# Kernel optimization log

Hardware: AMD Instinct MI355X
Metric: run time of the kernel (lower is better)

The kernel has to match this reference:

```python
import itertools
import jax, jax.numpy as jnp
import numpy as np

B, RES, RES_, STRIDE = 512, 14, 7, 2
IN_DIM, OUT_DIM, KEY_DIM, H, ATTN_RATIO = 256, 512, 16, 8, 2
NH_KD = KEY_DIM * H          # 128
D = ATTN_RATIO * KEY_DIM     # 32
DH = D * H                   # 256
KV_OUT = DH + NH_KD          # 384
N, N_ = RES * RES, RES_ * RES_   # 196, 49
EPS = 1e-5
SCALE = KEY_DIM ** -0.5


def _build_bias_idxs():
    points = list(itertools.product(range(RES), range(RES)))
    points_ = list(itertools.product(range(RES_), range(RES_)))
    offsets, idxs = {}, []
    for p1 in points_:
        for p2 in points:
            off = (abs(p1[0] * STRIDE - p2[0]), abs(p1[1] * STRIDE - p2[1]))
            if off not in offsets:
                offsets[off] = len(offsets)
            idxs.append(offsets[off])
    return np.array(idxs, dtype=np.int32).reshape(N_, N), len(offsets)


def _bn(x, g, b, m, v):
    # inference-mode BatchNorm1d over last dim
    return (x - m) * (g * jax.lax.rsqrt(v + EPS)) + b


def _hardswish(x):
    return x * jnp.clip(x + 3.0, 0.0, 6.0) * (1.0 / 6.0)


def setup_inputs() -> dict:
    key = jax.random.key(0)
    ks = jax.random.split(key, 16)
    idxs_np, n_off = _build_bias_idxs()
    inp = {
        "x": jax.random.normal(ks[0], (B, N, IN_DIM), jnp.float32),
        "w_kv": jax.random.normal(ks[1], (KV_OUT, IN_DIM), jnp.float32) * 0.02,
        "kv_g": jnp.ones((KV_OUT,), jnp.float32),
        "kv_b": jax.random.normal(ks[2], (KV_OUT,), jnp.float32) * 0.01,
        "kv_m": jax.random.normal(ks[3], (KV_OUT,), jnp.float32) * 0.01,
        "kv_v": jax.random.uniform(ks[4], (KV_OUT,), jnp.float32) + 0.5,
        "w_q": jax.random.normal(ks[5], (NH_KD, IN_DIM), jnp.float32) * 0.02,
        "q_g": jnp.ones((NH_KD,), jnp.float32),
        "q_b": jax.random.normal(ks[6], (NH_KD,), jnp.float32) * 0.01,
        "q_m": jax.random.normal(ks[7], (NH_KD,), jnp.float32) * 0.01,
        "q_v": jax.random.uniform(ks[8], (NH_KD,), jnp.float32) + 0.5,
        "w_p": jax.random.normal(ks[9], (OUT_DIM, DH), jnp.float32) * 0.02,
        "p_g": jnp.ones((OUT_DIM,), jnp.float32),
        "p_b": jax.random.normal(ks[10], (OUT_DIM,), jnp.float32) * 0.01,
        "p_m": jax.random.normal(ks[11], (OUT_DIM,), jnp.float32) * 0.01,
        "p_v": jax.random.uniform(ks[12], (OUT_DIM,), jnp.float32) + 0.5,
        "ab_table": jax.random.normal(ks[13], (H, n_off), jnp.float32) * 0.02,
        "bias_idxs": jnp.asarray(idxs_np),  # [N_, N] int32
    }
    return inp


def reference(x, w_kv, kv_g, kv_b, kv_m, kv_v,
              w_q, q_g, q_b, q_m, q_v,
              w_p, p_g, p_b, p_m, p_v,
              ab_table, bias_idxs):
    Bx = x.shape[0]
    # kv projection: [B, N, KV_OUT] -> split heads into k [B,H,N,KEY_DIM], v [B,H,N,D]
    kv = _bn(jnp.einsum('bnc,oc->bno', x, w_kv), kv_g, kv_b, kv_m, kv_v)
    kv = kv.reshape(Bx, N, H, KEY_DIM + D)
    k = kv[..., :KEY_DIM].transpose(0, 2, 1, 3)   # [B,H,N,KEY_DIM]
    v = kv[..., KEY_DIM:].transpose(0, 2, 1, 3)   # [B,H,N,D]
    # query path: spatial subsample then Linear+BN
    xs = x.reshape(Bx, RES, RES, IN_DIM)[:, ::STRIDE, ::STRIDE].reshape(Bx, N_, IN_DIM)
    q = _bn(jnp.einsum('bnc,oc->bno', xs, w_q), q_g, q_b, q_m, q_v)
    q = q.reshape(Bx, N_, H, KEY_DIM).transpose(0, 2, 1, 3)  # [B,H,N_,KEY_DIM]
    # relative-position bias gather: [H, N_, N]
    ab = ab_table[:, bias_idxs]
    attn = jnp.einsum('bhqd,bhkd->bhqk', q, k) * SCALE + ab
    attn = jax.nn.softmax(attn, axis=-1)
    out = jnp.einsum('bhqk,bhkd->bhqd', attn, v)           # [B,H,N_,D]
    out = out.transpose(0, 2, 1, 3).reshape(Bx, N_, DH)
    out = _hardswish(out)
    out = _bn(jnp.einsum('bnd,od->bno', out, w_p), p_g, p_b, p_m, p_v)
    return out
```

## Files before the change

### kernel.cpp

```cpp
#include <hip/hip_runtime.h>

typedef __attribute__((ext_vector_type(8))) short bf16x8;
typedef __attribute__((ext_vector_type(4))) float f32x4;
typedef __attribute__((ext_vector_type(4))) short short4v;
typedef __attribute__((ext_vector_type(4))) unsigned int u32x4;

#define DEVFN static __device__ __forceinline__

DEVFN short f2bf(float f) {
  unsigned int u = __builtin_bit_cast(unsigned int, f);
  unsigned int r = (u + 0x7FFFu + ((u >> 16) & 1u)) >> 16;
  return (short)r;
}

DEVFN unsigned int pack2bf(float a, float b) {
  unsigned int lo = (unsigned int)(unsigned short)f2bf(a);
  unsigned int hi = (unsigned int)(unsigned short)f2bf(b);
  return lo | (hi << 16);
}

DEVFN f32x4 mfma_bf16(bf16x8 a, bf16x8 b, f32x4 c) {
  return __builtin_amdgcn_mfma_f32_16x16x32_bf16(a, b, c, 0, 0, 0);
}

DEVFN f32x4 zero4() { f32x4 z = {0.f, 0.f, 0.f, 0.f}; return z; }
DEVFN bf16x8 zero8() { bf16x8 z = {0,0,0,0,0,0,0,0}; return z; }

DEVFN bf16x8 lds8(const short* p) {
  short4v lo = *reinterpret_cast<const short4v*>(p);
  short4v hi = *reinterpret_cast<const short4v*>(p + 4);
  bf16x8 r;
  r[0] = lo[0]; r[1] = lo[1]; r[2] = lo[2]; r[3] = lo[3];
  r[4] = hi[0]; r[5] = hi[1]; r[6] = hi[2]; r[7] = hi[3];
  return r;
}

__global__ void pack_w_k(const float* __restrict__ w, const float* __restrict__ g,
                         const float* __restrict__ b, const float* __restrict__ m,
                         const float* __restrict__ v, short* __restrict__ pk,
                         float* __restrict__ bias, int O) {
  const int t = blockIdx.x * 256 + threadIdx.x;
  const int nt = O >> 4;
  const int total = nt * 8 * 64;
  if (t < total) {
    int lane = t & 63;
    int j = (t >> 6) % nt;
    int c = (t >> 6) / nt;
    int row = j * 16 + (lane & 15);
    int col = c * 32 + (lane >> 4) * 8;
    float s = g[row] * rsqrtf(v[row] + 1e-5f);
    const float* wp = w + (size_t)row * 256 + col;
    short* o = pk + (size_t)t * 8;
#pragma unroll
    for (int e = 0; e < 8; ++e) o[e] = f2bf(wp[e] * s);
  }
  if (t < O) {
    float s = g[t] * rsqrtf(v[t] + 1e-5f);
    bias[t] = b[t] - m[t] * s;
  }
}

__global__ void ab_gather_k(const float* __restrict__ tab,
                            const int* __restrict__ idxs,
                            float* __restrict__ out, int n_off) {
  const int hq = blockIdx.x;
  const int h = hq / 49, q = hq % 49;
  const int t = threadIdx.x;
  if (t < 196)
    out[(size_t)hq * 196 + t] = tab[h * n_off + idxs[q * 196 + t]];
}

__global__ __launch_bounds__(256, 1) void fused_k(
    const float* __restrict__ x,
    const short* __restrict__ pkv, const float* __restrict__ bkv,
    const short* __restrict__ pq,  const float* __restrict__ bq_,
    const short* __restrict__ pp,  const float* __restrict__ bp_,
    const float* __restrict__ ab,  float* __restrict__ out) {
  __shared__ short lds[79984];
  short* xs  = lds;
  short* ks  = lds + 50176;
  short* vs  = lds + 54096;
  short* qs  = lds + 60400;
  short* as_ = lds + 66672;

  const int b = blockIdx.x;
  const int tid = threadIdx.x, w = tid >> 6, lane = tid & 63;
  const int l15 = lane & 15, g = lane >> 4;

  if (tid < 32) vs[6272 + tid] = 0;
  const float* xb = x + (size_t)b * 196 * 256;
  for (int i = tid; i < 6272; i += 256) {
    int row = i >> 5, gc = i & 31;
    const float* src = xb + row * 256 + gc * 8;
    float4 u0 = *reinterpret_cast<const float4*>(src);
    float4 u1 = *reinterpret_cast<const float4*>(src + 4);
    bf16x8 vv;
    vv[0] = f2bf(u0.x); vv[1] = f2bf(u0.y); vv[2] = f2bf(u0.z); vv[3] = f2bf(u0.w);
    vv[4] = f2bf(u1.x); vv[5] = f2bf(u1.y); vv[6] = f2bf(u1.z); vv[7] = f2bf(u1.w);
    int ob = (gc * 16) ^ ((row & 7) << 4);
    *reinterpret_cast<bf16x8*>(reinterpret_cast<char*>(xs) + row * 512 + ob) = vv;
  }
  __syncthreads();

#define XFRAG(row, c)                                                         \
  (*reinterpret_cast<const bf16x8*>(                                          \
      reinterpret_cast<const char*>(xs) + (row) * 512 +                       \
      (((c) * 64 + g * 16) ^ (((row) & 7) << 4))))

  {
    f32x4 qa[4][2];
#pragma unroll
    for (int mt = 0; mt < 4; ++mt) { qa[mt][0] = zero4(); qa[mt][1] = zero4(); }
#pragma unroll
    for (int c = 0; c < 8; ++c) {
      bf16x8 w0 = *reinterpret_cast<const bf16x8*>(pq + ((size_t)(c * 8 + 2 * w) * 64 + lane) * 8);
      bf16x8 w1 = *reinterpret_cast<const bf16x8*>(pq + ((size_t)(c * 8 + 2 * w + 1) * 64 + lane) * 8);
#pragma unroll
      for (int mt = 0; mt < 4; ++mt) {
        int qi = mt * 16 + l15; if (qi > 48) qi = 48;
        int xr = 28 * (qi / 7) + 2 * (qi % 7);
        bf16x8 a = XFRAG(xr, c);
        qa[mt][0] = mfma_bf16(a, w0, qa[mt][0]);
        qa[mt][1] = mfma_bf16(a, w1, qa[mt][1]);
      }
    }
#pragma unroll
    for (int mt = 0; mt < 4; ++mt) {
#pragma unroll
      for (int jj = 0; jj < 2; ++jj) {
        int ch = (2 * w + jj) * 16 + l15;
        float bv = bq_[ch];
#pragma unroll
        for (int r = 0; r < 4; ++r) {
          int q = mt * 16 + g * 4 + r;
          if (q < 49)
            *reinterpret_cast<short*>(reinterpret_cast<char*>(qs) + q * 256 +
                                      ((ch * 2) ^ ((q & 7) << 4))) =
                f2bf(qa[mt][jj][r] + bv);
        }
      }
    }
  }
  __syncthreads();

  for (int h = 0; h < 8; ++h) {
    {
      bf16x8 wf0[8], wf1[8], wf2[8];
#pragma unroll
      for (int c = 0; c < 8; ++c) {
        wf0[c] = *reinterpret_cast<const bf16x8*>(pkv + ((size_t)(c * 24 + 3 * h) * 64 + lane) * 8);
        wf1[c] = *reinterpret_cast<const bf16x8*>(pkv + ((size_t)(c * 24 + 3 * h + 1) * 64 + lane) * 8);
        wf2[c] = *reinterpret_cast<const bf16x8*>(pkv + ((size_t)(c * 24 + 3 * h + 2) * 64 + lane) * 8);
      }
      float bvK = bkv[3 * h * 16 + l15];
      float4 bv0 = *reinterpret_cast<const float4*>(bkv + (3 * h + 1) * 16 + g * 4);
      float4 bv1 = *reinterpret_cast<const float4*>(bkv + (3 * h + 2) * 16 + g * 4);
#pragma unroll
      for (int ti = 0; ti < 4; ++ti) {
        const int mt = (ti < 3) ? (w + ti * 4) : 12;
        const bool active = (ti < 3) || (w == 0);
        if (active) {
          f32x4 aK = zero4(), a0 = zero4(), a1 = zero4();
          int xr = mt * 16 + l15; if (xr > 195) xr = 195;
#pragma unroll
          for (int c = 0; c < 8; ++c) {
            bf16x8 a = XFRAG(xr, c);
            aK = mfma_bf16(a, wf0[c], aK);
            a0 = mfma_bf16(wf1[c], a, a0);
            a1 = mfma_bf16(wf2[c], a, a1);
          }
#pragma unroll
          for (int r = 0; r < 4; ++r) {
            int n = mt * 16 + g * 4 + r;
            if (n < 196) ks[n * 20 + l15] = f2bf(aK[r] + bvK);
          }
          int nv = mt * 16 + l15;
          if (nv < 196) {
#pragma unroll
            for (int r = 0; r < 4; ++r)
              vs[(g * 4 + r) * 196 + nv] = f2bf(a0[r] + bv0[r]);
#pragma unroll
            for (int r = 0; r < 4; ++r)
              vs[(16 + g * 4 + r) * 196 + nv] = f2bf(a1[r] + bv1[r]);
          }
        }
      }
    }
    __syncthreads();

    {
      int qm = w * 16 + l15; if (qm > 48) qm = 48;
      bf16x8 bq = zero8();
      if (g < 2)
        bq = *reinterpret_cast<const bf16x8*>(
            reinterpret_cast<const char*>(qs) + qm * 256 +
            ((h * 32 + g * 16) ^ ((qm & 7) << 4)));

      f32x4 s[13];
#pragma unroll
      for (int t = 0; t < 13; ++t) {
        int n_a = (t >> 1) * 32 + (l15 >> 2) * 8 + (t & 1) * 4 + (l15 & 3);
        bf16x8 ak = zero8();
        if (g < 2 && n_a < 196) ak = lds8(ks + n_a * 20 + g * 8);
        s[t] = mfma_bf16(ak, bq, zero4());
      }

      const float* abrow = ab + ((size_t)h * 49 + qm) * 196;
#pragma unroll
      for (int t = 0; t < 13; ++t) {
        int nb = (t >> 1) * 32 + g * 8 + (t & 1) * 4;
        if (nb < 196) {
          const float4 bi = *reinterpret_cast<const float4*>(abrow + nb);
          s[t][0] = s[t][0] * 0.25f + bi.x;
          s[t][1] = s[t][1] * 0.25f + bi.y;
          s[t][2] = s[t][2] * 0.25f + bi.z;
          s[t][3] = s[t][3] * 0.25f + bi.w;
        } else {
          s[t][0] = -1e30f; s[t][1] = -1e30f; s[t][2] = -1e30f; s[t][3] = -1e30f;
        }
      }

      float mx = s[0][0];
#pragma unroll
      for (int t = 0; t < 13; ++t)
        mx = fmaxf(mx, fmaxf(fmaxf(s[t][0], s[t][1]), fmaxf(s[t][2], s[t][3])));
      mx = fmaxf(mx, __shfl_xor(mx, 16, 64));
      mx = fmaxf(mx, __shfl_xor(mx, 32, 64));
      float sum = 0.f;
#pragma unroll
      for (int t = 0; t < 13; ++t) {
#pragma unroll
        for (int r = 0; r < 4; ++r) {
          float e = __expf(s[t][r] - mx);
          s[t][r] = e;
          sum += e;
        }
      }
      sum += __shfl_xor(sum, 16, 64);
      sum += __shfl_xor(sum, 32, 64);
      const float inv = 1.f / sum;

      unsigned int pkr[14][2];
#pragma unroll
      for (int t = 0; t < 13; ++t) {
        pkr[t][0] = pack2bf(s[t][0] * inv, s[t][1] * inv);
        pkr[t][1] = pack2bf(s[t][2] * inv, s[t][3] * inv);
      }
      pkr[13][0] = 0u; pkr[13][1] = 0u;

      f32x4 o0 = zero4(), o1 = zero4();
#pragma unroll
      for (int c = 0; c < 7; ++c) {
        u32x4 bp_u;
        bp_u[0] = pkr[2 * c][0];     bp_u[1] = pkr[2 * c][1];
        bp_u[2] = pkr[2 * c + 1][0]; bp_u[3] = pkr[2 * c + 1][1];
        bf16x8 bp = __builtin_bit_cast(bf16x8, bp_u);
        bf16x8 v0 = lds8(vs + l15 * 196 + c * 32 + g * 8);
        bf16x8 v1 = lds8(vs + (16 + l15) * 196 + c * 32 + g * 8);
        o0 = mfma_bf16(bp, v0, o0);
        o1 = mfma_bf16(bp, v1, o1);
      }

#pragma unroll
      for (int r = 0; r < 4; ++r) {
        int q2 = w * 16 + g * 4 + r;
        if (q2 < 52) {
          float x0 = o0[r];
          float h0 = x0 * fminf(fmaxf(x0 + 3.f, 0.f), 6.f) * (1.f / 6.f);
          float x1 = o1[r];
          float h1 = x1 * fminf(fmaxf(x1 + 3.f, 0.f), 6.f) * (1.f / 6.f);
          char* base = reinterpret_cast<char*>(as_) + q2 * 512;
          int sw = (q2 & 7) << 4;
          *reinterpret_cast<short*>(base + ((h * 64 + l15 * 2) ^ sw)) = f2bf(h0);
          *reinterpret_cast<short*>(base + ((h * 64 + 32 + l15 * 2) ^ sw)) = f2bf(h1);
        }
      }
    }
    __syncthreads();
  }

  {
    f32x4 pa[4][8];
#pragma unroll
    for (int mt = 0; mt < 4; ++mt)
#pragma unroll
      for (int j = 0; j < 8; ++j) pa[mt][j] = zero4();

#pragma unroll
    for (int c = 0; c < 8; ++c) {
      bf16x8 wp[8];
#pragma unroll
      for (int j = 0; j < 8; ++j)
        wp[j] = *reinterpret_cast<const bf16x8*>(pp + ((size_t)(c * 32 + w * 8 + j) * 64 + lane) * 8);
#pragma unroll
      for (int mt = 0; mt < 4; ++mt) {
        int rb = (mt < 3) ? mt * 16 : 36;
        int row = rb + l15;
        bf16x8 a = *reinterpret_cast<const bf16x8*>(
            reinterpret_cast<const char*>(as_) + row * 512 +
            ((c * 64 + g * 16) ^ ((row & 7) << 4)));
#pragma unroll
        for (int j = 0; j < 8; ++j) pa[mt][j] = mfma_bf16(a, wp[j], pa[mt][j]);
      }
    }

#pragma unroll
    for (int mt = 0; mt < 4; ++mt) {
      int rb = (mt < 3) ? mt * 16 : 36;
#pragma unroll
      for (int j = 0; j < 8; ++j) {
        float bv = bp_[w * 128 + j * 16 + l15];
#pragma unroll
        for (int r = 0; r < 4; ++r) {
          int q2 = rb + g * 4 + r;
          if (q2 < 49 && (mt < 3 || q2 >= 48))
            out[((size_t)b * 49 + q2) * 512 + w * 128 + j * 16 + l15] =
                pa[mt][j][r] + bv;
        }
      }
    }
  }
#undef XFRAG
}

extern "C" void kernel_launch(void* const* d_in, const int* in_sizes, int n_in,
                              void* d_out, int out_size, void* d_ws, size_t ws_size,
                              hipStream_t stream) {
  const float* x    = (const float*)d_in[0];
  const float* w_kv = (const float*)d_in[1];
  const float* kv_g = (const float*)d_in[2];
  const float* kv_b = (const float*)d_in[3];
  const float* kv_m = (const float*)d_in[4];
  const float* kv_v = (const float*)d_in[5];
  const float* w_q  = (const float*)d_in[6];
  const float* q_g  = (const float*)d_in[7];
  const float* q_b  = (const float*)d_in[8];
  const float* q_m  = (const float*)d_in[9];
  const float* q_v  = (const float*)d_in[10];
  const float* w_p  = (const float*)d_in[11];
  const float* p_g  = (const float*)d_in[12];
  const float* p_b  = (const float*)d_in[13];
  const float* p_m  = (const float*)d_in[14];
  const float* p_v  = (const float*)d_in[15];
  const float* ab_t = (const float*)d_in[16];
  const int*   idxs = (const int*)d_in[17];
  const int n_off = in_sizes[16] / 8;

  char* ws = (char*)d_ws;
  short* pk_kv = (short*)(ws);
  short* pk_q  = (short*)(ws + 196608);
  short* pk_p  = (short*)(ws + 262144);
  float* bs_kv = (float*)(ws + 524288);
  float* bs_q  = (float*)(ws + 525824);
  float* bs_p  = (float*)(ws + 526336);
  float* ab_ws = (float*)(ws + 528384);

  pack_w_k<<<dim3(48), dim3(256), 0, stream>>>(w_kv, kv_g, kv_b, kv_m, kv_v, pk_kv, bs_kv, 384);
  pack_w_k<<<dim3(16), dim3(256), 0, stream>>>(w_q, q_g, q_b, q_m, q_v, pk_q, bs_q, 128);
  pack_w_k<<<dim3(64), dim3(256), 0, stream>>>(w_p, p_g, p_b, p_m, p_v, pk_p, bs_p, 512);
  ab_gather_k<<<dim3(392), dim3(256), 0, stream>>>(ab_t, idxs, ab_ws, n_off);

  fused_k<<<dim3(512), dim3(256), 0, stream>>>(
      x, pk_kv, bs_kv, pk_q, bs_q, pk_p, bs_p, ab_ws, (float*)d_out);
}
```

Baseline: 142.0 us.

## Warp-specialize attention kernel with double-buffered KV and split out projection GEMM

The fused kernel now runs 512 threads. Four producer waves compute the KV projection for the next head into a double buffer while four consumer waves run attention on the current head, so the two stages overlap instead of running back to back. The final projection is moved into a separate GEMM kernel that streams weights into LDS with global_load_lds, and the hardswish attention output goes through a bf16 workspace in global memory. The V rows are padded to 198 elements, presumably to reduce LDS bank conflicts. This adds a global round trip and an extra launch, and occupancy is bounded by about 154KB of LDS per block.

```diff
diff --git a/kernel.cpp b/kernel.cpp
--- a/kernel.cpp
+++ b/kernel.cpp
@@ -25,6 +25,12 @@
 
 DEVFN f32x4 zero4() { f32x4 z = {0.f, 0.f, 0.f, 0.f}; return z; }
 DEVFN bf16x8 zero8() { bf16x8 z = {0,0,0,0,0,0,0,0}; return z; }
+
+DEVFN void gload_lds16(const void* g, void* l) {
+  __builtin_amdgcn_global_load_lds(
+      (const __attribute__((address_space(1))) unsigned int*)g,
+      (__attribute__((address_space(3))) unsigned int*)l, 16, 0, 0);
+}
 
 DEVFN bf16x8 lds8(const short* p) {
   short4v lo = *reinterpret_cast<const short4v*>(p);
@@ -70,26 +76,33 @@
     out[(size_t)hq * 196 + t] = tab[h * n_off + idxs[q * 196 + t]];
 }
 
-__global__ __launch_bounds__(256, 1) void fused_k(
+__global__ __launch_bounds__(512, 2) void fused2_k(
     const float* __restrict__ x,
     const short* __restrict__ pkv, const float* __restrict__ bkv,
     const short* __restrict__ pq,  const float* __restrict__ bq_,
-    const short* __restrict__ pp,  const float* __restrict__ bp_,
-    const float* __restrict__ ab,  float* __restrict__ out) {
-  __shared__ short lds[79984];
-  short* xs  = lds;
-  short* ks  = lds + 50176;
-  short* vs  = lds + 54096;
-  short* qs  = lds + 60400;
-  short* as_ = lds + 66672;
+    const float* __restrict__ ab,  short* __restrict__ at_out) {
+  __shared__ short lds[77024];
+  short* xs   = lds;
+  short* qs   = lds + 50176;
+  short* ksb0 = lds + 56448;
+  short* ksb1 = lds + 60368;
+  short* vsb0 = lds + 64288;
+  short* vsb1 = lds + 70656;
 
   const int b = blockIdx.x;
-  const int tid = threadIdx.x, w = tid >> 6, lane = tid & 63;
+  const int tid = threadIdx.x, wid = tid >> 6, lane = tid & 63;
   const int l15 = lane & 15, g = lane >> 4;
 
-  if (tid < 32) vs[6272 + tid] = 0;
+  if (tid < 32) vsb0[6336 + tid] = 0;
+  else if (tid < 64) vsb1[6336 + (tid - 32)] = 0;
+  else if (tid < 192) {
+    int i = tid - 64;
+    short* vb = (i < 64) ? vsb0 : vsb1;
+    int row = (i >> 1) & 31;
+    vb[row * 198 + 196 + (i & 1)] = 0;
+  }
   const float* xb = x + (size_t)b * 196 * 256;
-  for (int i = tid; i < 6272; i += 256) {
+  for (int i = tid; i < 6272; i += 512) {
     int row = i >> 5, gc = i & 31;
     const float* src = xb + row * 256 + gc * 8;
     float4 u0 = *reinterpret_cast<const float4*>(src);
@@ -107,14 +120,145 @@
       reinterpret_cast<const char*>(xs) + (row) * 512 +                       \
       (((c) * 64 + g * 16) ^ (((row) & 7) << 4))))
 
-  {
+  auto kv_head = [&](int hh, short* ksd, short* vsd) {
+    const int pw = wid - 4;
+    bf16x8 wf0[8], wf1[8], wf2[8];
+#pragma unroll
+    for (int c = 0; c < 8; ++c) {
+      wf0[c] = *reinterpret_cast<const bf16x8*>(pkv + ((size_t)(c * 24 + 3 * hh) * 64 + lane) * 8);
+      wf1[c] = *reinterpret_cast<const bf16x8*>(pkv + ((size_t)(c * 24 + 3 * hh + 1) * 64 + lane) * 8);
+      wf2[c] = *reinterpret_cast<const bf16x8*>(pkv + ((size_t)(c * 24 + 3 * hh + 2) * 64 + lane) * 8);
+    }
+    float  bvK = bkv[3 * hh * 16 + l15];
+    float4 bv0 = *reinterpret_cast<const float4*>(bkv + (3 * hh + 1) * 16 + g * 4);
+    float4 bv1 = *reinterpret_cast<const float4*>(bkv + (3 * hh + 2) * 16 + g * 4);
+#pragma unroll
+    for (int ti = 0; ti < 4; ++ti) {
+      const int tile = pw + ti * 4;
+      if (tile < 13) {
+        f32x4 aK = zero4(), a0 = zero4(), a1 = zero4();
+        int xr = tile * 16 + l15; if (xr > 195) xr = 195;
+#pragma unroll
+        for (int c = 0; c < 8; ++c) {
+          bf16x8 a = XFRAG(xr, c);
+          aK = mfma_bf16(a, wf0[c], aK);
+          a0 = mfma_bf16(wf1[c], a, a0);
+          a1 = mfma_bf16(wf2[c], a, a1);
+        }
+#pragma unroll
+        for (int r = 0; r < 4; ++r) {
+          int n = tile * 16 + g * 4 + r;
+          if (n < 196) ksd[n * 20 + l15] = f2bf(aK[r] + bvK);
+        }
+        int nv = tile * 16 + l15;
+        if (nv < 196) {
+#pragma unroll
+          for (int r = 0; r < 4; ++r)
+            vsd[(g * 4 + r) * 198 + nv] = f2bf(a0[r] + bv0[r]);
+#pragma unroll
+          for (int r = 0; r < 4; ++r)
+            vsd[(16 + g * 4 + r) * 198 + nv] = f2bf(a1[r] + bv1[r]);
+        }
+      }
+    }
+  };
+
+  auto attn_head = [&](int hh, const short* ksd, const short* vsd) {
+    int qm = wid * 16 + l15; if (qm > 48) qm = 48;
+    bf16x8 bq = zero8();
+    if (g < 2)
+      bq = *reinterpret_cast<const bf16x8*>(
+          reinterpret_cast<const char*>(qs) + qm * 256 +
+          ((hh * 32 + g * 16) ^ ((qm & 7) << 4)));
+
+    f32x4 s[13];
+#pragma unroll
+    for (int t = 0; t < 13; ++t) {
+      int n_a = (t >> 1) * 32 + (l15 >> 2) * 8 + (t & 1) * 4 + (l15 & 3);
+      bf16x8 ak = zero8();
+      if (g < 2 && n_a < 196) ak = lds8(ksd + n_a * 20 + g * 8);
+      s[t] = mfma_bf16(ak, bq, zero4());
+    }
+
+    const float* abrow = ab + ((size_t)hh * 49 + qm) * 196;
+#pragma unroll
+    for (int t = 0; t < 13; ++t) {
+      int nb = (t >> 1) * 32 + g * 8 + (t & 1) * 4;
+      if (nb < 196) {
+        const float4 bi = *reinterpret_cast<const float4*>(abrow + nb);
+        s[t][0] = s[t][0] * 0.25f + bi.x;
+        s[t][1] = s[t][1] * 0.25f + bi.y;
+        s[t][2] = s[t][2] * 0.25f + bi.z;
+        s[t][3] = s[t][3] * 0.25f + bi.w;
+      } else {
+        s[t][0] = -1e30f; s[t][1] = -1e30f; s[t][2] = -1e30f; s[t][3] = -1e30f;
+      }
+    }
+
+    float mx = s[0][0];
+#pragma unroll
+    for (int t = 0; t < 13; ++t)
+      mx = fmaxf(mx, fmaxf(fmaxf(s[t][0], s[t][1]), fmaxf(s[t][2], s[t][3])));
+    mx = fmaxf(mx, __shfl_xor(mx, 16, 64));
+    mx = fmaxf(mx, __shfl_xor(mx, 32, 64));
+    float sum = 0.f;
+#pragma unroll
+    for (int t = 0; t < 13; ++t) {
+#pragma unroll
+      for (int r = 0; r < 4; ++r) {
+        float e = __expf(s[t][r] - mx);
+        s[t][r] = e;
+        sum += e;
+      }
+    }
+    sum += __shfl_xor(sum, 16, 64);
+    sum += __shfl_xor(sum, 32, 64);
+    const float inv = 1.f / sum;
+
+    unsigned int pkr[14][2];
+#pragma unroll
+    for (int t = 0; t < 13; ++t) {
+      pkr[t][0] = pack2bf(s[t][0] * inv, s[t][1] * inv);
+      pkr[t][1] = pack2bf(s[t][2] * inv, s[t][3] * inv);
+    }
+    pkr[13][0] = 0u; pkr[13][1] = 0u;
+
+    f32x4 o0 = zero4(), o1 = zero4();
+#pragma unroll
+    for (int c = 0; c < 7; ++c) {
+      u32x4 bp_u;
+      bp_u[0] = pkr[2 * c][0];     bp_u[1] = pkr[2 * c][1];
+      bp_u[2] = pkr[2 * c + 1][0]; bp_u[3] = pkr[2 * c + 1][1];
+      bf16x8 bp = __builtin_bit_cast(bf16x8, bp_u);
+      bf16x8 v0 = lds8(vsd + l15 * 198 + c * 32 + g * 8);
+      bf16x8 v1 = lds8(vsd + (16 + l15) * 198 + c * 32 + g * 8);
+      o0 = mfma_bf16(bp, v0, o0);
+      o1 = mfma_bf16(bp, v1, o1);
+    }
+
+#pragma unroll
+    for (int r = 0; r < 4; ++r) {
+      int q2 = wid * 16 + g * 4 + r;
+      if (q2 < 49) {
+        float x0 = o0[r];
+        float h0 = x0 * fminf(fmaxf(x0 + 3.f, 0.f), 6.f) * (1.f / 6.f);
+        float x1 = o1[r];
+        float h1 = x1 * fminf(fmaxf(x1 + 3.f, 0.f), 6.f) * (1.f / 6.f);
+        short* op = at_out + ((size_t)b * 49 + q2) * 256 + hh * 32;
+        op[l15] = f2bf(h0);
+        op[16 + l15] = f2bf(h1);
+      }
+    }
+  };
+
+  if (wid < 4) {
     f32x4 qa[4][2];
 #pragma unroll
     for (int mt = 0; mt < 4; ++mt) { qa[mt][0] = zero4(); qa[mt][1] = zero4(); }
 #pragma unroll
     for (int c = 0; c < 8; ++c) {
-      bf16x8 w0 = *reinterpret_cast<const bf16x8*>(pq + ((size_t)(c * 8 + 2 * w) * 64 + lane) * 8);
-      bf16x8 w1 = *reinterpret_cast<const bf16x8*>(pq + ((size_t)(c * 8 + 2 * w + 1) * 64 + lane) * 8);
+      bf16x8 w0 = *reinterpret_cast<const bf16x8*>(pq + ((size_t)(c * 8 + 2 * wid) * 64 + lane) * 8);
+      bf16x8 w1 = *reinterpret_cast<const bf16x8*>(pq + ((size_t)(c * 8 + 2 * wid + 1) * 64 + lane) * 8);
 #pragma unroll
       for (int mt = 0; mt < 4; ++mt) {
         int qi = mt * 16 + l15; if (qi > 48) qi = 48;
@@ -128,199 +272,75 @@
     for (int mt = 0; mt < 4; ++mt) {
 #pragma unroll
       for (int jj = 0; jj < 2; ++jj) {
-        int ch = (2 * w + jj) * 16 + l15;
+        int ch = (2 * wid + jj) * 16 + l15;
         float bv = bq_[ch];
 #pragma unroll
         for (int r = 0; r < 4; ++r) {
-          int q = mt * 16 + g * 4 + r;
-          if (q < 49)
-            *reinterpret_cast<short*>(reinterpret_cast<char*>(qs) + q * 256 +
-                                      ((ch * 2) ^ ((q & 7) << 4))) =
+          int qq = mt * 16 + g * 4 + r;
+          if (qq < 49)
+            *reinterpret_cast<short*>(reinterpret_cast<char*>(qs) + qq * 256 +
+                                      ((ch * 2) ^ ((qq & 7) << 4))) =
                 f2bf(qa[mt][jj][r] + bv);
         }
       }
     }
+  } else {
+    kv_head(0, ksb0, vsb0);
   }
   __syncthreads();
 
+#pragma unroll 1
   for (int h = 0; h < 8; ++h) {
-    {
-      bf16x8 wf0[8], wf1[8], wf2[8];
-#pragma unroll
-      for (int c = 0; c < 8; ++c) {
-        wf0[c] = *reinterpret_cast<const bf16x8*>(pkv + ((size_t)(c * 24 + 3 * h) * 64 + lane) * 8);
-        wf1[c] = *reinterpret_cast<const bf16x8*>(pkv + ((size_t)(c * 24 + 3 * h + 1) * 64 + lane) * 8);
-        wf2[c] = *reinterpret_cast<const bf16x8*>(pkv + ((size_t)(c * 24 + 3 * h + 2) * 64 + lane) * 8);
-      }
-      float bvK = bkv[3 * h * 16 + l15];
-      float4 bv0 = *reinterpret_cast<const float4*>(bkv + (3 * h + 1) * 16 + g * 4);
-      float4 bv1 = *reinterpret_cast<const float4*>(bkv + (3 * h + 2) * 16 + g * 4);
-#pragma unroll
-      for (int ti = 0; ti < 4; ++ti) {
-        const int mt = (ti < 3) ? (w + ti * 4) : 12;
-        const bool active = (ti < 3) || (w == 0);
-        if (active) {
-          f32x4 aK = zero4(), a0 = zero4(), a1 = zero4();
-          int xr = mt * 16 + l15; if (xr > 195) xr = 195;
-#pragma unroll
-          for (int c = 0; c < 8; ++c) {
-            bf16x8 a = XFRAG(xr, c);
-            aK = mfma_bf16(a, wf0[c], aK);
-            a0 = mfma_bf16(wf1[c], a, a0);
-            a1 = mfma_bf16(wf2[c], a, a1);
-          }
-#pragma unroll
-          for (int r = 0; r < 4; ++r) {
-            int n = mt * 16 + g * 4 + r;
-            if (n < 196) ks[n * 20 + l15] = f2bf(aK[r] + bvK);
-          }
-          int nv = mt * 16 + l15;
-          if (nv < 196) {
-#pragma unroll
-            for (int r = 0; r < 4; ++r)
-              vs[(g * 4 + r) * 196 + nv] = f2bf(a0[r] + bv0[r]);
-#pragma unroll
-            for (int r = 0; r < 4; ++r)
-              vs[(16 + g * 4 + r) * 196 + nv] = f2bf(a1[r] + bv1[r]);
-          }
-        }
-      }
+    if (wid < 4) {
+      attn_head(h, (h & 1) ? ksb1 : ksb0, (h & 1) ? vsb1 : vsb0);
+    } else if (h < 7) {
+      kv_head(h + 1, (h & 1) ? ksb0 : ksb1, (h & 1) ? vsb0 : vsb1);
     }
     __syncthreads();
-
-    {
-      int qm = w * 16 + l15; if (qm > 48) qm = 48;
-      bf16x8 bq = zero8();
-      if (g < 2)
-        bq = *reinterpret_cast<const bf16x8*>(
-            reinterpret_cast<const char*>(qs) + qm * 256 +
-            ((h * 32 + g * 16) ^ ((qm & 7) << 4)));
-
-      f32x4 s[13];
-#pragma unroll
-      for (int t = 0; t < 13; ++t) {
-        int n_a = (t >> 1) * 32 + (l15 >> 2) * 8 + (t & 1) * 4 + (l15 & 3);
-        bf16x8 ak = zero8();
-        if (g < 2 && n_a < 196) ak = lds8(ks + n_a * 20 + g * 8);
-        s[t] = mfma_bf16(ak, bq, zero4());
-      }
-
-      const float* abrow = ab + ((size_t)h * 49 + qm) * 196;
-#pragma unroll
-      for (int t = 0; t < 13; ++t) {
-        int nb = (t >> 1) * 32 + g * 8 + (t & 1) * 4;
-        if (nb < 196) {
-          const float4 bi = *reinterpret_cast<const float4*>(abrow + nb);
-          s[t][0] = s[t][0] * 0.25f + bi.x;
-          s[t][1] = s[t][1] * 0.25f + bi.y;
-          s[t][2] = s[t][2] * 0.25f + bi.z;
-          s[t][3] = s[t][3] * 0.25f + bi.w;
-        } else {
-          s[t][0] = -1e30f; s[t][1] = -1e30f; s[t][2] = -1e30f; s[t][3] = -1e30f;
-        }
-      }
-
-      float mx = s[0][0];
-#pragma unroll
-      for (int t = 0; t < 13; ++t)
-        mx = fmaxf(mx, fmaxf(fmaxf(s[t][0], s[t][1]), fmaxf(s[t][2], s[t][3])));
-      mx = fmaxf(mx, __shfl_xor(mx, 16, 64));
-      mx = fmaxf(mx, __shfl_xor(mx, 32, 64));
-      float sum = 0.f;
-#pragma unroll
-      for (int t = 0; t < 13; ++t) {
-#pragma unroll
-        for (int r = 0; r < 4; ++r) {
-          float e = __expf(s[t][r] - mx);
-          s[t][r] = e;
-          sum += e;
-        }
-      }
-      sum += __shfl_xor(sum, 16, 64);
-      sum += __shfl_xor(sum, 32, 64);
-      const float inv = 1.f / sum;
-
-      unsigned int pkr[14][2];
-#pragma unroll
-      for (int t = 0; t < 13; ++t) {
-        pkr[t][0] = pack2bf(s[t][0] * inv, s[t][1] * inv);
-        pkr[t][1] = pack2bf(s[t][2] * inv, s[t][3] * inv);
-      }
-      pkr[13][0] = 0u; pkr[13][1] = 0u;
-
-      f32x4 o0 = zero4(), o1 = zero4();
-#pragma unroll
-      for (int c = 0; c < 7; ++c) {
-        u32x4 bp_u;
-        bp_u[0] = pkr[2 * c][0];     bp_u[1] = pkr[2 * c][1];
-        bp_u[2] = pkr[2 * c + 1][0]; bp_u[3] = pkr[2 * c + 1][1];
-        bf16x8 bp = __builtin_bit_cast(bf16x8, bp_u);
-        bf16x8 v0 = lds8(vs + l15 * 196 + c * 32 + g * 8);
-        bf16x8 v1 = lds8(vs + (16 + l15) * 196 + c * 32 + g * 8);
-        o0 = mfma_bf16(bp, v0, o0);
-        o1 = mfma_bf16(bp, v1, o1);
-      }
-
-#pragma unroll
-      for (int r = 0; r < 4; ++r) {
-        int q2 = w * 16 + g * 4 + r;
-        if (q2 < 52) {
-          float x0 = o0[r];
-          float h0 = x0 * fminf(fmaxf(x0 + 3.f, 0.f), 6.f) * (1.f / 6.f);
-          float x1 = o1[r];
-          float h1 = x1 * fminf(fmaxf(x1 + 3.f, 0.f), 6.f) * (1.f / 6.f);
-          char* base = reinterpret_cast<char*>(as_) + q2 * 512;
-          int sw = (q2 & 7) << 4;
-          *reinterpret_cast<short*>(base + ((h * 64 + l15 * 2) ^ sw)) = f2bf(h0);
-          *reinterpret_cast<short*>(base + ((h * 64 + 32 + l15 * 2) ^ sw)) = f2bf(h1);
-        }
-      }
-    }
+  }
+#undef XFRAG
+}
+
+__global__ __launch_bounds__(256) void p_gemm2(
+    const short* __restrict__ a_in, const short* __restrict__ pk,
+    const float* __restrict__ bias, float* __restrict__ out) {
+  __shared__ short bs[16 * 512];
+  __shared__ float sb[256];
+  const int tid = threadIdx.x, w_id = tid >> 6, lane = tid & 63;
+  const int l15 = lane & 15, gq = lane >> 4;
+  const int half = blockIdx.x & 1;
+  const int mt = blockIdx.x >> 1;
+  for (int i = tid; i < 256; i += 256) sb[i] = bias[half * 256 + i];
+  const int arow = mt * 64 + w_id * 16 + l15;
+  const short* arp = a_in + (size_t)arow * 256;
+
+  f32x4 acc[16];
+#pragma unroll
+  for (int j = 0; j < 16; ++j) acc[j] = zero4();
+
+  for (int c = 0; c < 8; ++c) {
+    for (int seg = w_id; seg < 16; seg += 4)
+      gload_lds16(pk + ((size_t)(c * 32 + half * 16 + seg) * 64 + lane) * 8,
+                  &bs[seg * 512]);
+    bf16x8 a = *reinterpret_cast<const bf16x8*>(arp + c * 32 + gq * 8);
     __syncthreads();
-  }
-
-  {
-    f32x4 pa[4][8];
-#pragma unroll
-    for (int mt = 0; mt < 4; ++mt)
-#pragma unroll
-      for (int j = 0; j < 8; ++j) pa[mt][j] = zero4();
-
-#pragma unroll
-    for (int c = 0; c < 8; ++c) {
-      bf16x8 wp[8];
-#pragma unroll
-      for (int j = 0; j < 8; ++j)
-        wp[j] = *reinterpret_cast<const bf16x8*>(pp + ((size_t)(c * 32 + w * 8 + j) * 64 + lane) * 8);
-#pragma unroll
-      for (int mt = 0; mt < 4; ++mt) {
-        int rb = (mt < 3) ? mt * 16 : 36;
-        int row = rb + l15;
-        bf16x8 a = *reinterpret_cast<const bf16x8*>(
-            reinterpret_cast<const char*>(as_) + row * 512 +
-            ((c * 64 + g * 16) ^ ((row & 7) << 4)));
-#pragma unroll
-        for (int j = 0; j < 8; ++j) pa[mt][j] = mfma_bf16(a, wp[j], pa[mt][j]);
-      }
-    }
-
-#pragma unroll
-    for (int mt = 0; mt < 4; ++mt) {
-      int rb = (mt < 3) ? mt * 16 : 36;
-#pragma unroll
-      for (int j = 0; j < 8; ++j) {
-        float bv = bp_[w * 128 + j * 16 + l15];
-#pragma unroll
-        for (int r = 0; r < 4; ++r) {
-          int q2 = rb + g * 4 + r;
-          if (q2 < 49 && (mt < 3 || q2 >= 48))
-            out[((size_t)b * 49 + q2) * 512 + w * 128 + j * 16 + l15] =
-                pa[mt][j][r] + bv;
-        }
-      }
-    }
-  }
-#undef XFRAG
+#pragma unroll
+    for (int j = 0; j < 16; ++j) {
+      bf16x8 bj = *reinterpret_cast<const bf16x8*>(&bs[(j * 64 + lane) * 8]);
+      acc[j] = mfma_bf16(a, bj, acc[j]);
+    }
+    __syncthreads();
+  }
+  const int orow = mt * 64 + w_id * 16 + gq * 4;
+#pragma unroll
+  for (int j = 0; j < 16; ++j) {
+    int chl = j * 16 + l15;
+    float bb = sb[chl];
+    int och = half * 256 + chl;
+#pragma unroll
+    for (int r = 0; r < 4; ++r)
+      out[(size_t)(orow + r) * 512 + och] = acc[j][r] + bb;
+  }
 }
 
 extern "C" void kernel_launch(void* const* d_in, const int* in_sizes, int n_in,
@@ -354,12 +374,14 @@
   float* bs_q  = (float*)(ws + 525824);
   float* bs_p  = (float*)(ws + 526336);
   float* ab_ws = (float*)(ws + 528384);
+  short* at_ws = (short*)(ws + 835712);
 
   pack_w_k<<<dim3(48), dim3(256), 0, stream>>>(w_kv, kv_g, kv_b, kv_m, kv_v, pk_kv, bs_kv, 384);
   pack_w_k<<<dim3(16), dim3(256), 0, stream>>>(w_q, q_g, q_b, q_m, q_v, pk_q, bs_q, 128);
   pack_w_k<<<dim3(64), dim3(256), 0, stream>>>(w_p, p_g, p_b, p_m, p_v, pk_p, bs_p, 512);
   ab_gather_k<<<dim3(392), dim3(256), 0, stream>>>(ab_t, idxs, ab_ws, n_off);
 
-  fused_k<<<dim3(512), dim3(256), 0, stream>>>(
-      x, pk_kv, bs_kv, pk_q, bs_q, pk_p, bs_p, ab_ws, (float*)d_out);
-}
+  fused2_k<<<dim3(512), dim3(512), 0, stream>>>(
+      x, pk_kv, bs_kv, pk_q, bs_q, ab_ws, at_ws);
+  p_gemm2<<<dim3(784), dim3(256), 0, stream>>>(at_ws, pk_p, bs_p, (float*)d_out);
+}
```

New measurement: 160.2 us. 12.8% more time.
